# Kernel tuning notes

Hardware: AMD Instinct MI355X
Metric: run time of the kernel (lower is better)

The kernel has to match this reference:

```python
import jax, jax.numpy as jnp
import numpy as np

N_NODES = 50000
N_EDGES = 800000
D_FEAT = 128
DIM = 3
IN_CH = DIM + 2 * D_FEAT  # 259
HID = 256
OUT = 128


def setup_inputs() -> dict:
    key = jax.random.key(0)
    ks = jax.random.split(key, 10)
    x = jax.random.normal(ks[0], (N_NODES, D_FEAT), dtype=jnp.float32)
    pos = jax.random.normal(ks[1], (N_NODES, DIM), dtype=jnp.float32)
    edge_index = jax.random.randint(ks[2], (2, N_EDGES), 0, N_NODES, dtype=jnp.int64)
    s0 = 1.0 / np.sqrt(IN_CH)
    s2 = 1.0 / np.sqrt(HID)
    W0 = jax.random.uniform(ks[3], (HID, IN_CH), jnp.float32, -s0, s0)
    b0 = jax.random.uniform(ks[4], (HID,), jnp.float32, -s0, s0)
    W2 = jax.random.uniform(ks[5], (HID, HID), jnp.float32, -s2, s2)
    b2 = jax.random.uniform(ks[6], (HID,), jnp.float32, -s2, s2)
    W3 = jax.random.uniform(ks[7], (OUT, HID), jnp.float32, -s2, s2)
    b3 = jax.random.uniform(ks[8], (OUT,), jnp.float32, -s2, s2)
    return {"x": x, "edge_index": edge_index, "pos": pos,
            "W0": W0, "b0": b0, "W2": W2, "b2": b2, "W3": W3, "b3": b3}


def reference(x, edge_index, pos, W0, b0, W2, b2, W3, b3):
    src, dst = edge_index[0], edge_index[1]
    edge_attr = pos[dst] - pos[src]              # [E, 3]
    node_i = x[src]                              # [E, D]
    node_j = x[dst]                              # [E, D]
    inp = jnp.concatenate((edge_attr, node_i, node_j), axis=1)  # [E, 259]
    h = jax.nn.elu(inp @ W0.T + b0)
    h = jax.nn.elu(h @ W2.T + b2)
    return h @ W3.T + b3                         # [E, 128]
```

## Files before the change

kernel.cpp:

```cpp
#include <hip/hip_runtime.h>
#include <cstddef>
#include <cstdint>


#define N_NODES_C 50000
#define N_EDGES_C 800000
#define D_FEAT_C  128
#define IN_CH_C   259
#define HID_C     256
#define OUT_CH_C  128

#define BM8    64
#define HSTR8  272
#define SW(row, c) ((c) ^ (((row) & 7) << 3))

typedef unsigned short u16;
typedef short bf16x8 __attribute__((ext_vector_type(8)));
typedef float f32x4 __attribute__((ext_vector_type(4)));

__device__ __forceinline__ u16 f2bf(float f) {
    union { float f; unsigned u; } v; v.f = f;
    unsigned u = v.u;
    return (u16)((u + 0x7fffu + ((u >> 16) & 1u)) >> 16);
}
__device__ __forceinline__ unsigned cvt_pk_bf16(float lo, float hi) {
    unsigned r;
    asm("v_cvt_pk_bf16_f32 %0, %1, %2" : "=v"(r) : "v"(lo), "v"(hi));
    return r;
}
__device__ __forceinline__ float bf2f_lo(unsigned u) {
    union { unsigned u; float f; } v; v.u = u << 16; return v.f;
}
__device__ __forceinline__ float bf2f_hi(unsigned u) {
    union { unsigned u; float f; } v; v.u = u & 0xFFFF0000u; return v.f;
}
__device__ __forceinline__ float elu1(float x) {
    return x > 0.0f ? x : (__expf(x) - 1.0f);
}
__device__ __forceinline__ unsigned addelu_pk(unsigned a, unsigned b) {
    float s0 = elu1(bf2f_lo(a) + bf2f_lo(b));
    float s1 = elu1(bf2f_hi(a) + bf2f_hi(b));
    return cvt_pk_bf16(s0, s1);
}

__global__ void detect_idx64(const void* __restrict__ ei_raw, int* __restrict__ flag) {
    if (blockIdx.x == 0 && threadIdx.x == 0) {
        const unsigned long long* p = (const unsigned long long*)ei_raw;
        int is64 = 1;
        for (int i = 0; i < 64; ++i)
            if (p[i] >= (1ULL << 32)) { is64 = 0; break; }
        *flag = is64;
    }
}

__global__ void prep_weights(const float* __restrict__ W0, const float* __restrict__ W2,
                             const float* __restrict__ W3, u16* __restrict__ WAB,
                             u16* __restrict__ W2f, u16* __restrict__ W3f) {
    int i = blockIdx.x * blockDim.x + threadIdx.x;
    const int nwab = 512 * 160, nw2 = 256 * 256, nw3 = 128 * 256;
    if (i < nwab) {
        int j = i / 160, k = i - j * 160;
        float v = 0.f;
        if (j < 256) {
            if (k < 128) v = W0[j * IN_CH_C + 3 + k];
            else if (k < 131) v = -W0[j * IN_CH_C + (k - 128)];
        } else {
            int j2 = j - 256;
            if (k < 128) v = W0[j2 * IN_CH_C + 131 + k];
            else if (k < 131) v = W0[j2 * IN_CH_C + (k - 128)];
        }
        WAB[i] = f2bf(v);
    } else if (i < nwab + nw2) {
        int q = i - nwab;
        int c = q & 7, lIdx = (q >> 3) & 63, kk = (q >> 9) & 7, jb = q >> 12;
        int j = jb * 16 + (lIdx & 15);
        int k = kk * 32 + ((lIdx >> 4) << 3) + c;
        W2f[q] = f2bf(W2[j * 256 + k]);
    } else if (i < nwab + nw2 + nw3) {
        int q = i - nwab - nw2;
        int c = q & 7, lIdx = (q >> 3) & 63, kk = (q >> 9) & 7, ob = q >> 12;
        int o = ob * 16 + (lIdx & 15);
        int k = kk * 32 + ((lIdx >> 4) << 3) + c;
        W3f[q] = f2bf(W3[o * 256 + k]);
    }
}

extern "C" __global__ void __launch_bounds__(512, 2)
node_gemm(const float* __restrict__ x, const float* __restrict__ pos,
          const u16* __restrict__ WAB, const float* __restrict__ b0,
          u16* __restrict__ AB) {
    __shared__ u16 tile[128 * 168];
    const int t = threadIdx.x;
    const int row0 = blockIdx.x * 128;
    for (int idx = t; idx < 128 * 80; idx += 512) {
        int m = idx / 80, wq = idx - m * 80;
        int k = wq * 2, n = row0 + m;
        float f0 = 0.f, f1 = 0.f;
        if (n < N_NODES_C) {
            f0 = (k < 128) ? x[(size_t)n * 128 + k] : (k < 131 ? pos[(size_t)n * 3 + k - 128] : 0.f);
            int k1 = k + 1;
            f1 = (k1 < 128) ? x[(size_t)n * 128 + k1] : (k1 < 131 ? pos[(size_t)n * 3 + k1 - 128] : 0.f);
        }
        *(unsigned*)&tile[m * 168 + k] = (unsigned)f2bf(f0) | ((unsigned)f2bf(f1) << 16);
    }
    __syncthreads();
    const int w = t >> 6, l = t & 63, lr = l & 15, hi = l >> 4;
    for (int mc = 0; mc < 2; ++mc) {
        f32x4 acc[4][4];
#pragma unroll
        for (int ji = 0; ji < 4; ++ji)
#pragma unroll
            for (int mi = 0; mi < 4; ++mi)
                acc[ji][mi] = (f32x4){0.f, 0.f, 0.f, 0.f};
#pragma unroll
        for (int kk = 0; kk < 5; ++kk) {
            bf16x8 af[4], bfr[4];
#pragma unroll
            for (int ji = 0; ji < 4; ++ji)
                af[ji] = *(const bf16x8*)&WAB[(size_t)(w * 64 + ji * 16 + lr) * 160 + kk * 32 + hi * 8];
#pragma unroll
            for (int mi = 0; mi < 4; ++mi)
                bfr[mi] = *(const bf16x8*)&tile[(mc * 64 + mi * 16 + lr) * 168 + kk * 32 + hi * 8];
#pragma unroll
            for (int ji = 0; ji < 4; ++ji)
#pragma unroll
                for (int mi = 0; mi < 4; ++mi)
                    acc[ji][mi] = __builtin_amdgcn_mfma_f32_16x16x32_bf16(af[ji], bfr[mi], acc[ji][mi], 0, 0, 0);
        }
#pragma unroll
        for (int ji = 0; ji < 4; ++ji) {
            int j0 = w * 64 + ji * 16 + hi * 4;
            float4 bb = make_float4(0.f, 0.f, 0.f, 0.f);
            if (j0 < 256) bb = *(const float4*)&b0[j0];
#pragma unroll
            for (int mi = 0; mi < 4; ++mi) {
                int nn = row0 + mc * 64 + mi * 16 + lr;
                if (nn < N_NODES_C) {
                    f32x4 v = acc[ji][mi];
                    uint2 pr;
                    pr.x = cvt_pk_bf16(v[0] + bb.x, v[1] + bb.y);
                    pr.y = cvt_pk_bf16(v[2] + bb.z, v[3] + bb.w);
                    *(uint2*)&AB[(size_t)nn * 512 + j0] = pr;
                }
            }
        }
    }
}

extern "C" __global__ void __launch_bounds__(512, 4)
edge_mlp_v8(const u16* __restrict__ AB, const void* __restrict__ ei_raw,
            const int* __restrict__ idx64_flag,
            const u16* __restrict__ W2f, const float* __restrict__ b2,
            const u16* __restrict__ W3f, const float* __restrict__ b3,
            float* __restrict__ out) {
    __shared__ u16 h1[BM8 * HSTR8];
    __shared__ u16 h2[BM8 * HSTR8];

    const int t = threadIdx.x;
    const int e0 = blockIdx.x * BM8;
    const int w = t >> 6, l = t & 63, lr = l & 15, hi = l >> 4;

    {
        const int m = t >> 3, q = t & 7;
        const int eid = e0 + m;
        int sA, sB;
        if (*idx64_flag) {
            const long long* e = (const long long*)ei_raw;
            sA = (int)e[eid]; sB = (int)e[N_EDGES_C + eid];
        } else {
            const int* e = (const int*)ei_raw;
            sA = e[eid]; sB = e[N_EDGES_C + eid];
        }
        const u16* ra = AB + (size_t)sA * 512 + q * 32;
        const u16* rb = AB + (size_t)sB * 512 + 256 + q * 32;
        uint4 a[4], b[4];
#pragma unroll
        for (int i = 0; i < 4; ++i) a[i] = *(const uint4*)(ra + i * 8);
#pragma unroll
        for (int i = 0; i < 4; ++i) b[i] = *(const uint4*)(rb + i * 8);
#pragma unroll
        for (int i = 0; i < 4; ++i) {
            uint4 r;
            r.x = addelu_pk(a[i].x, b[i].x);
            r.y = addelu_pk(a[i].y, b[i].y);
            r.z = addelu_pk(a[i].z, b[i].z);
            r.w = addelu_pk(a[i].w, b[i].w);
            *(uint4*)&h1[m * HSTR8 + SW(m, q * 32 + i * 8)] = r;
        }
    }
    __syncthreads();

    f32x4 acc[2][4];
#pragma unroll
    for (int ji = 0; ji < 2; ++ji) {
        const float4 bb = *(const float4*)&b2[w * 32 + ji * 16 + hi * 4];
#pragma unroll
        for (int mi = 0; mi < 4; ++mi)
            acc[ji][mi] = (f32x4){bb.x, bb.y, bb.z, bb.w};
    }
    __builtin_amdgcn_s_setprio(1);
#pragma unroll
    for (int kk = 0; kk < 8; ++kk) {
        bf16x8 af[2], bfr[4];
#pragma unroll
        for (int ji = 0; ji < 2; ++ji)
            af[ji] = *(const bf16x8*)&W2f[(size_t)(((w * 2 + ji) * 8 + kk) * 64 + l) * 8];
#pragma unroll
        for (int mi = 0; mi < 4; ++mi) {
            int row = mi * 16 + lr;
            bfr[mi] = *(const bf16x8*)&h1[row * HSTR8 + SW(row, kk * 32 + hi * 8)];
        }
#pragma unroll
        for (int ji = 0; ji < 2; ++ji)
#pragma unroll
            for (int mi = 0; mi < 4; ++mi)
                acc[ji][mi] = __builtin_amdgcn_mfma_f32_16x16x32_bf16(af[ji], bfr[mi], acc[ji][mi], 0, 0, 0);
    }
    __builtin_amdgcn_s_setprio(0);

#pragma unroll
    for (int ji = 0; ji < 2; ++ji) {
        int j0 = w * 32 + ji * 16 + hi * 4;
#pragma unroll
        for (int mi = 0; mi < 4; ++mi) {
            int mm = mi * 16 + lr;
            f32x4 v = acc[ji][mi];
            uint2 pr;
            pr.x = cvt_pk_bf16(elu1(v[0]), elu1(v[1]));
            pr.y = cvt_pk_bf16(elu1(v[2]), elu1(v[3]));
            *(uint2*)&h2[mm * HSTR8 + SW(mm, j0)] = pr;
        }
    }
    __syncthreads();

    f32x4 acc2[4];
    {
        const float4 bv = *(const float4*)&b3[w * 16 + hi * 4];
#pragma unroll
        for (int mi = 0; mi < 4; ++mi)
            acc2[mi] = (f32x4){bv.x, bv.y, bv.z, bv.w};
    }
    __builtin_amdgcn_s_setprio(1);
#pragma unroll
    for (int kk = 0; kk < 8; ++kk) {
        bf16x8 af3, bh[4];
        af3 = *(const bf16x8*)&W3f[(size_t)((w * 8 + kk) * 64 + l) * 8];
#pragma unroll
        for (int mi = 0; mi < 4; ++mi) {
            int row = mi * 16 + lr;
            bh[mi] = *(const bf16x8*)&h2[row * HSTR8 + SW(row, kk * 32 + hi * 8)];
        }
#pragma unroll
        for (int mi = 0; mi < 4; ++mi)
            acc2[mi] = __builtin_amdgcn_mfma_f32_16x16x32_bf16(af3, bh[mi], acc2[mi], 0, 0, 0);
    }
    __builtin_amdgcn_s_setprio(0);

#pragma unroll
    for (int mi = 0; mi < 4; ++mi) {
        f32x4 v = acc2[mi];
        float4 o4;
        o4.x = v[0]; o4.y = v[1]; o4.z = v[2]; o4.w = v[3];
        *(float4*)&out[(size_t)(e0 + mi * 16 + lr) * 128 + w * 16 + hi * 4] = o4;
    }
}

#define BM 64
#define PAD 65
__global__ void transpose_f32(const float* __restrict__ src, float* __restrict__ dst, int R, int C) {
    int i = blockIdx.x * blockDim.x + threadIdx.x;
    if (i < R * C) { int c = i / R; int r = i - c * R; dst[i] = src[r * C + c]; }
}
__device__ __forceinline__ void layer256(const float* __restrict__ wt, const float* __restrict__ b,
                                         const float* in_lds, float* out_lds, int K, int t) {
    const int jg = t & 63, mc = t >> 6;
    const float* wp = wt + jg * 4;
    const float4 bv = *(const float4*)&b[jg * 4];
    float acc[8][4];
#pragma unroll
    for (int i = 0; i < 8; ++i) { acc[i][0] = bv.x; acc[i][1] = bv.y; acc[i][2] = bv.z; acc[i][3] = bv.w; }
    const float* hbase = in_lds + mc * 8;
    float4 wv = *(const float4*)wp;
    for (int k = 0; k < K; ++k) {
        float4 wn = wv;
        if (k + 1 < K) wn = *(const float4*)(wp + (size_t)(k + 1) * HID_C);
        float h[8];
#pragma unroll
        for (int i = 0; i < 8; ++i) h[i] = hbase[k * PAD + i];
#pragma unroll
        for (int i = 0; i < 8; ++i) {
            acc[i][0] += h[i] * wv.x; acc[i][1] += h[i] * wv.y;
            acc[i][2] += h[i] * wv.z; acc[i][3] += h[i] * wv.w;
        }
        wv = wn;
    }
#pragma unroll
    for (int i4 = 0; i4 < 4; ++i4)
#pragma unroll
        for (int i = 0; i < 8; ++i) {
            float v = acc[i][i4];
            v = v > 0.0f ? v : expm1f(v);
            out_lds[(jg * 4 + i4) * PAD + mc * 8 + i] = v;
        }
}
extern "C" __global__ void __launch_bounds__(512, 2)
edge_mlp_f32(const float* __restrict__ x, const void* __restrict__ ei_raw,
             const float* __restrict__ pos, const int* __restrict__ idx64_flag,
             const float* __restrict__ wt0, const float* __restrict__ b0,
             const float* __restrict__ wt2, const float* __restrict__ b2,
             const float* __restrict__ wt3, const float* __restrict__ b3,
             float* __restrict__ out) {
    __shared__ float buf1[IN_CH_C * PAD];
    __shared__ float buf2[HID_C * PAD];
    __shared__ int s_src[BM], s_dst[BM];
    const int t = threadIdx.x;
    const int e0 = blockIdx.x * BM;
    if (t < BM) {
        int s, d;
        if (*idx64_flag) {
            const long long* e = (const long long*)ei_raw;
            s = (int)e[e0 + t]; d = (int)e[N_EDGES_C + e0 + t];
        } else {
            const int* e = (const int*)ei_raw;
            s = e[e0 + t]; d = e[N_EDGES_C + e0 + t];
        }
        s_src[t] = s; s_dst[t] = d;
    }
    __syncthreads();
    if (t < BM) {
        const int s = s_src[t], d = s_dst[t];
#pragma unroll
        for (int i = 0; i < 3; ++i)
            buf1[i * PAD + t] = pos[d * 3 + i] - pos[s * 3 + i];
    }
    {
        const int l = t & 31, grp = t >> 5;
#pragma unroll
        for (int r = 0; r < 4; ++r) {
            const int m = grp + r * 16;
            const int s = s_src[m], d = s_dst[m];
            const float4 xi = *(const float4*)&x[(size_t)s * D_FEAT_C + l * 4];
            const float4 xj = *(const float4*)&x[(size_t)d * D_FEAT_C + l * 4];
            buf1[(3 + l * 4 + 0) * PAD + m] = xi.x; buf1[(3 + l * 4 + 1) * PAD + m] = xi.y;
            buf1[(3 + l * 4 + 2) * PAD + m] = xi.z; buf1[(3 + l * 4 + 3) * PAD + m] = xi.w;
            buf1[(131 + l * 4 + 0) * PAD + m] = xj.x; buf1[(131 + l * 4 + 1) * PAD + m] = xj.y;
            buf1[(131 + l * 4 + 2) * PAD + m] = xj.z; buf1[(131 + l * 4 + 3) * PAD + m] = xj.w;
        }
    }
    __syncthreads();
    layer256(wt0, b0, buf1, buf2, IN_CH_C, t);
    __syncthreads();
    layer256(wt2, b2, buf2, buf1, HID_C, t);
    __syncthreads();
    {
        const int jg = t & 31, mc = t >> 5;
        const float* wp = wt3 + jg * 4;
        const float4 bv = *(const float4*)&b3[jg * 4];
        float acc[4][4];
#pragma unroll
        for (int i = 0; i < 4; ++i) { acc[i][0] = bv.x; acc[i][1] = bv.y; acc[i][2] = bv.z; acc[i][3] = bv.w; }
        const float* hbase = buf1 + mc * 4;
        float4 wv = *(const float4*)wp;
        for (int k = 0; k < HID_C; ++k) {
            float4 wn = wv;
            if (k + 1 < HID_C) wn = *(const float4*)(wp + (size_t)(k + 1) * OUT_CH_C);
            float h[4];
#pragma unroll
            for (int i = 0; i < 4; ++i) h[i] = hbase[k * PAD + i];
#pragma unroll
            for (int i = 0; i < 4; ++i) {
                acc[i][0] += h[i] * wv.x; acc[i][1] += h[i] * wv.y;
                acc[i][2] += h[i] * wv.z; acc[i][3] += h[i] * wv.w;
            }
            wv = wn;
        }
#pragma unroll
        for (int i = 0; i < 4; ++i) {
            float4 o;
            o.x = acc[i][0]; o.y = acc[i][1]; o.z = acc[i][2]; o.w = acc[i][3];
            *(float4*)&out[(size_t)(e0 + mc * 4 + i) * OUT_CH_C + jg * 4] = o;
        }
    }
}

extern "C" void kernel_launch(void* const* d_in, const int* in_sizes, int n_in,
                              void* d_out, int out_size, void* d_ws, size_t ws_size,
                              hipStream_t stream) {
    const float* x   = (const float*)d_in[0];
    const void*  ei  = d_in[1];
    const float* pos = (const float*)d_in[2];
    const float* W0  = (const float*)d_in[3];
    const float* b0  = (const float*)d_in[4];
    const float* W2  = (const float*)d_in[5];
    const float* b2  = (const float*)d_in[6];
    const float* W3  = (const float*)d_in[7];
    const float* b3  = (const float*)d_in[8];
    float* out = (float*)d_out;

    const size_t need = (size_t)N_NODES_C * 512 * 2 + (size_t)512 * 160 * 2
                      + (size_t)256 * 256 * 2 + (size_t)128 * 256 * 2 + 16;
    if (ws_size >= need) {
        u16* AB  = (u16*)d_ws;
        u16* WAB = AB + (size_t)N_NODES_C * 512;
        u16* W2f = WAB + 512 * 160;
        u16* W3f = W2f + 256 * 256;
        int* flag = (int*)(W3f + 128 * 256);

        detect_idx64<<<1, 64, 0, stream>>>(ei, flag);
        prep_weights<<<704, 256, 0, stream>>>(W0, W2, W3, WAB, W2f, W3f);
        node_gemm<<<391, 512, 0, stream>>>(x, pos, WAB, b0, AB);
        edge_mlp_v8<<<N_EDGES_C / BM8, 512, 0, stream>>>(AB, ei, flag, W2f, b2, W3f, b3, out);
    } else {
        float* wt0 = (float*)d_ws;
        float* wt2 = wt0 + IN_CH_C * HID_C;
        float* wt3 = wt2 + HID_C * HID_C;
        int*   flag = (int*)(wt3 + HID_C * OUT_CH_C);

        detect_idx64<<<1, 64, 0, stream>>>(ei, flag);
        int n0 = HID_C * IN_CH_C;
        transpose_f32<<<(n0 + 255) / 256, 256, 0, stream>>>(W0, wt0, HID_C, IN_CH_C);
        int n2 = HID_C * HID_C;
        transpose_f32<<<(n2 + 255) / 256, 256, 0, stream>>>(W2, wt2, HID_C, HID_C);
        int n3 = OUT_CH_C * HID_C;
        transpose_f32<<<(n3 + 255) / 256, 256, 0, stream>>>(W3, wt3, OUT_CH_C, HID_C);
        edge_mlp_f32<<<N_EDGES_C / BM, 512, 0, stream>>>(
            x, ei, pos, flag, wt0, b0, wt2, b2, wt3, b3, out);
    }
}
```

Measured before the change: 369.7 us.

## Bucket-sort edges by destination and remap workgroups per XCD for cache locality

Adds a counting sort of edges into 512 buckets keyed by destination node (histogram, scan, atomic scatter), then runs the edge MLP over the permuted edge order and scatters outputs back through the saved edge ids. Workgroup ids are remapped so each XCD processes a contiguous range of sorted edges, so destination-row gathers from the node table should hit the per-XCD L2. The LDS swizzle is replaced by a padded stride of 264. The sort costs several extra kernel launches, atomics and extra index traffic, and the output writes become scattered rows.

```diff
diff --git a/kernel.cpp b/kernel.cpp
--- a/kernel.cpp
+++ b/kernel.cpp
@@ -10,9 +10,12 @@
 #define HID_C     256
 #define OUT_CH_C  128
 
-#define BM8    64
-#define HSTR8  272
-#define SW(row, c) ((c) ^ (((row) & 7) << 3))
+#define BM11   64
+#define NWG11  (N_EDGES_C / BM11)
+#define NWGQ   1562
+#define NWGR   4
+#define HSTR11 264
+#define NBUCK  512
 
 typedef unsigned short u16;
 typedef short bf16x8 __attribute__((ext_vector_type(8)));
@@ -50,6 +53,50 @@
         for (int i = 0; i < 64; ++i)
             if (p[i] >= (1ULL << 32)) { is64 = 0; break; }
         *flag = is64;
+    }
+}
+
+__global__ void zero_hist(int* __restrict__ hist) {
+    if (threadIdx.x < NBUCK) hist[threadIdx.x] = 0;
+}
+__global__ void bucket_hist(const void* __restrict__ ei_raw, const int* __restrict__ flag,
+                            int* __restrict__ hist) {
+    int e = blockIdx.x * blockDim.x + threadIdx.x;
+    if (e < N_EDGES_C) {
+        int dst = *flag ? (int)((const long long*)ei_raw)[N_EDGES_C + e]
+                        : ((const int*)ei_raw)[N_EDGES_C + e];
+        atomicAdd(&hist[dst >> 7], 1);
+    }
+}
+__global__ void bucket_scan(const int* __restrict__ hist, int* __restrict__ cur) {
+    __shared__ int tmp[NBUCK];
+    const int t = threadIdx.x;
+    const int orig = hist[t];
+    tmp[t] = orig;
+    __syncthreads();
+    for (int off = 1; off < NBUCK; off <<= 1) {
+        int x = (t >= off) ? tmp[t - off] : 0;
+        __syncthreads();
+        tmp[t] += x;
+        __syncthreads();
+    }
+    cur[t] = tmp[t] - orig;
+}
+__global__ void bucket_scatter(const void* __restrict__ ei_raw, const int* __restrict__ flag,
+                               int* __restrict__ cur, int* __restrict__ srcP,
+                               int* __restrict__ dstP, int* __restrict__ eidP) {
+    int e = blockIdx.x * blockDim.x + threadIdx.x;
+    if (e < N_EDGES_C) {
+        int src, dst;
+        if (*flag) {
+            const long long* p = (const long long*)ei_raw;
+            src = (int)p[e]; dst = (int)p[N_EDGES_C + e];
+        } else {
+            const int* p = (const int*)ei_raw;
+            src = p[e]; dst = p[N_EDGES_C + e];
+        }
+        int pos = atomicAdd(&cur[dst >> 7], 1);
+        srcP[pos] = src; dstP[pos] = dst; eidP[pos] = e;
     }
 }
 
@@ -148,29 +195,26 @@
 }
 
 extern "C" __global__ void __launch_bounds__(512, 4)
-edge_mlp_v8(const u16* __restrict__ AB, const void* __restrict__ ei_raw,
-            const int* __restrict__ idx64_flag,
-            const u16* __restrict__ W2f, const float* __restrict__ b2,
-            const u16* __restrict__ W3f, const float* __restrict__ b3,
-            float* __restrict__ out) {
-    __shared__ u16 h1[BM8 * HSTR8];
-    __shared__ u16 h2[BM8 * HSTR8];
+edge_mlp_v11(const u16* __restrict__ AB,
+             const int* __restrict__ srcP, const int* __restrict__ dstP,
+             const int* __restrict__ eidP,
+             const u16* __restrict__ W2f, const float* __restrict__ b2,
+             const u16* __restrict__ W3f, const float* __restrict__ b3,
+             float* __restrict__ out) {
+    __shared__ u16 h1[BM11 * HSTR11];
+    __shared__ u16 h2[BM11 * HSTR11];
 
     const int t = threadIdx.x;
-    const int e0 = blockIdx.x * BM8;
+    const int orig = blockIdx.x;
+    const int xcd = orig & 7, oi8 = orig >> 3;
+    const int wg = (xcd < NWGR ? xcd * (NWGQ + 1) : NWGR * (NWGQ + 1) + (xcd - NWGR) * NWGQ) + oi8;
+    const int e0 = wg * BM11;
     const int w = t >> 6, l = t & 63, lr = l & 15, hi = l >> 4;
 
     {
         const int m = t >> 3, q = t & 7;
-        const int eid = e0 + m;
-        int sA, sB;
-        if (*idx64_flag) {
-            const long long* e = (const long long*)ei_raw;
-            sA = (int)e[eid]; sB = (int)e[N_EDGES_C + eid];
-        } else {
-            const int* e = (const int*)ei_raw;
-            sA = e[eid]; sB = e[N_EDGES_C + eid];
-        }
+        const int sA = srcP[e0 + m];
+        const int sB = dstP[e0 + m];
         const u16* ra = AB + (size_t)sA * 512 + q * 32;
         const u16* rb = AB + (size_t)sB * 512 + 256 + q * 32;
         uint4 a[4], b[4];
@@ -185,7 +229,7 @@
             r.y = addelu_pk(a[i].y, b[i].y);
             r.z = addelu_pk(a[i].z, b[i].z);
             r.w = addelu_pk(a[i].w, b[i].w);
-            *(uint4*)&h1[m * HSTR8 + SW(m, q * 32 + i * 8)] = r;
+            *(uint4*)&h1[m * HSTR11 + q * 32 + i * 8] = r;
         }
     }
     __syncthreads();
@@ -208,7 +252,7 @@
 #pragma unroll
         for (int mi = 0; mi < 4; ++mi) {
             int row = mi * 16 + lr;
-            bfr[mi] = *(const bf16x8*)&h1[row * HSTR8 + SW(row, kk * 32 + hi * 8)];
+            bfr[mi] = *(const bf16x8*)&h1[row * HSTR11 + kk * 32 + hi * 8];
         }
 #pragma unroll
         for (int ji = 0; ji < 2; ++ji)
@@ -228,7 +272,7 @@
             uint2 pr;
             pr.x = cvt_pk_bf16(elu1(v[0]), elu1(v[1]));
             pr.y = cvt_pk_bf16(elu1(v[2]), elu1(v[3]));
-            *(uint2*)&h2[mm * HSTR8 + SW(mm, j0)] = pr;
+            *(uint2*)&h2[mm * HSTR11 + j0] = pr;
         }
     }
     __syncthreads();
@@ -248,7 +292,7 @@
 #pragma unroll
         for (int mi = 0; mi < 4; ++mi) {
             int row = mi * 16 + lr;
-            bh[mi] = *(const bf16x8*)&h2[row * HSTR8 + SW(row, kk * 32 + hi * 8)];
+            bh[mi] = *(const bf16x8*)&h2[row * HSTR11 + kk * 32 + hi * 8];
         }
 #pragma unroll
         for (int mi = 0; mi < 4; ++mi)
@@ -258,10 +302,11 @@
 
 #pragma unroll
     for (int mi = 0; mi < 4; ++mi) {
+        const int eo = eidP[e0 + mi * 16 + lr];
         f32x4 v = acc2[mi];
         float4 o4;
         o4.x = v[0]; o4.y = v[1]; o4.z = v[2]; o4.w = v[3];
-        *(float4*)&out[(size_t)(e0 + mi * 16 + lr) * 128 + w * 16 + hi * 4] = o4;
+        *(float4*)&out[(size_t)eo * 128 + w * 16 + hi * 4] = o4;
     }
 }
 
@@ -398,18 +443,30 @@
     float* out = (float*)d_out;
 
     const size_t need = (size_t)N_NODES_C * 512 * 2 + (size_t)512 * 160 * 2
-                      + (size_t)256 * 256 * 2 + (size_t)128 * 256 * 2 + 16;
+                      + (size_t)256 * 256 * 2 + (size_t)128 * 256 * 2
+                      + (size_t)3 * N_EDGES_C * 4 + (1 + 2 * NBUCK) * 4 + 64;
     if (ws_size >= need) {
         u16* AB  = (u16*)d_ws;
         u16* WAB = AB + (size_t)N_NODES_C * 512;
         u16* W2f = WAB + 512 * 160;
         u16* W3f = W2f + 256 * 256;
-        int* flag = (int*)(W3f + 128 * 256);
+        int* srcP = (int*)(W3f + 128 * 256);
+        int* dstP = srcP + N_EDGES_C;
+        int* eidP = dstP + N_EDGES_C;
+        int* flag = eidP + N_EDGES_C;
+        int* hist = flag + 1;
+        int* cur  = hist + NBUCK;
 
         detect_idx64<<<1, 64, 0, stream>>>(ei, flag);
+        zero_hist<<<1, NBUCK, 0, stream>>>(hist);
+        bucket_hist<<<(N_EDGES_C + 255) / 256, 256, 0, stream>>>(ei, flag, hist);
+        bucket_scan<<<1, NBUCK, 0, stream>>>(hist, cur);
+        bucket_scatter<<<(N_EDGES_C + 255) / 256, 256, 0, stream>>>(ei, flag, cur,
+                                                                    srcP, dstP, eidP);
         prep_weights<<<704, 256, 0, stream>>>(W0, W2, W3, WAB, W2f, W3f);
         node_gemm<<<391, 512, 0, stream>>>(x, pos, WAB, b0, AB);
-        edge_mlp_v8<<<N_EDGES_C / BM8, 512, 0, stream>>>(AB, ei, flag, W2f, b2, W3f, b3, out);
+        edge_mlp_v11<<<NWG11, 512, 0, stream>>>(AB, srcP, dstP, eidP,
+                                                W2f, b2, W3f, b3, out);
     } else {
         float* wt0 = (float*)d_ws;
         float* wt2 = wt0 + IN_CH_C * HID_C;
```

Result: slower. 932.8 us (+152.3%).
